# Kernel optimization log

Measured on AMD Instinct MI355X. Metric: run time of the kernel, lower is better.

## Reference

```python
import jax, jax.numpy as jnp
import numpy as np

N, E, IN, H, OUT = 50000, 800000, 128, 128, 64
BN_EPS = 1e-5


def setup_inputs() -> dict:
    key = jax.random.key(0)
    ks = jax.random.split(key, 12)
    x = jax.random.normal(ks[0], (N, IN), dtype=jnp.float32)
    edge_index = jax.random.randint(ks[1], (2, E), 0, N, dtype=jnp.int32)
    def lin(k, fan_in, fan_out):
        s = 1.0 / np.sqrt(fan_in)
        return jax.random.uniform(k, (fan_in, fan_out), jnp.float32, -s, s)
    params = {
        'W1': lin(ks[2], IN, H),  'b1': jnp.zeros((H,), jnp.float32),
        'W2': lin(ks[3], H, H),   'b2': jnp.zeros((H,), jnp.float32),
        'W3': lin(ks[4], H, H),   'b3': jnp.zeros((H,), jnp.float32),
        'W4': lin(ks[5], H, OUT), 'b4': jnp.zeros((OUT,), jnp.float32),
        'g1': jnp.ones((H,), jnp.float32), 'be1': jnp.zeros((H,), jnp.float32),
        'g2': jnp.ones((H,), jnp.float32), 'be2': jnp.zeros((H,), jnp.float32),
        'g3': jnp.ones((H,), jnp.float32), 'be3': jnp.zeros((H,), jnp.float32),
    }
    return dict(x=x, edge_index=edge_index, **params)


def _gcn_conv(x, src, dst, dinv, norm, W, b):
    # GCNConv: symmetric-normalized aggregation with self loops.
    h = x @ W                                   # [N, F]
    agg = jax.ops.segment_sum(h[src] * norm[:, None], dst, num_segments=N)
    agg = agg + h * (dinv * dinv)[:, None]      # self-loop contribution
    return agg + b


def _bn(x, gamma, beta):
    mu = jnp.mean(x, axis=0)
    var = jnp.mean(jnp.square(x - mu), axis=0)
    return (x - mu) * jax.lax.rsqrt(var + BN_EPS) * gamma + beta


def reference(x, edge_index, W1, b1, W2, b2, W3, b3, W4, b4, g1, be1, g2, be2, g3, be3):
    src, dst = edge_index[0], edge_index[1]
    # degree with self loops; fixed by the graph, shared across layers
    deg = jax.ops.segment_sum(jnp.ones((E,), x.dtype), dst, num_segments=N) + 1.0
    dinv = jax.lax.rsqrt(deg)
    norm = dinv[src] * dinv[dst]                # [E]

    h = _gcn_conv(x, src, dst, dinv, norm, W1, b1)
    h = jax.nn.relu(_bn(h, g1, be1))
    h = _gcn_conv(h, src, dst, dinv, norm, W2, b2)
    h = jax.nn.relu(_bn(h, g2, be2))
    h = _gcn_conv(h, src, dst, dinv, norm, W3, b3)
    h = jax.nn.relu(_bn(h, g3, be3))
    return _gcn_conv(h, src, dst, dinv, norm, W4, b4)
```

## Files before the change

kernel.cpp:

```cpp
#include <hip/hip_runtime.h>

constexpr int NN = 50000;
constexpr int NE = 800000;
constexpr float EPS = 1e-5f;

constexpr int CAP     = 64;
constexpr int FILL_NB = (NE + 255) / 256;
constexpr int WCONV_NB = (57344 + 255) / 256;

typedef short bf16x8 __attribute__((ext_vector_type(8)));
typedef float f32x4  __attribute__((ext_vector_type(4)));

__device__ __forceinline__ ushort f2bf(float x) {
    union { float f; unsigned u; } a; a.f = x;
    unsigned u = a.u;
    unsigned r = (u + 0x7FFFu + ((u >> 16) & 1u)) >> 16;
    return (ushort)r;
}
__device__ __forceinline__ float bflo(unsigned p) {
    union { unsigned u; float f; } a; a.u = p << 16; return a.f;
}
__device__ __forceinline__ float bfhi(unsigned p) {
    union { unsigned u; float f; } a; a.u = p & 0xFFFF0000u; return a.f;
}

__global__ void fillwconv_kernel(const int* __restrict__ src, const int* __restrict__ dst,
                                 int* __restrict__ curA, int* __restrict__ curB,
                                 ushort* __restrict__ csrf,
                                 const float* __restrict__ W1, const float* __restrict__ W2,
                                 const float* __restrict__ W3, const float* __restrict__ W4,
                                 ushort* __restrict__ Wt) {
    if (blockIdx.x < FILL_NB) {
        int e = blockIdx.x * 256 + threadIdx.x;
        if (e < NE) {
            int d = dst[e];
            if (e < NE / 2) {
                int slot = atomicAdd(&curA[d], 1);
                if (slot < CAP) csrf[(size_t)d * CAP + slot] = (ushort)src[e];
            } else {
                int old = atomicAdd(&curB[d], 1);
                int slot = CAP - 1 - old;
                if (slot >= 0) csrf[(size_t)d * CAP + slot] = (ushort)src[e];
            }
        }
    } else {
        int id = (blockIdx.x - FILL_NB) * 256 + threadIdx.x;
        if (id < 49152) {
            int l = id / 16384, r = id % 16384;
            int n = r >> 7, k = r & 127;
            const float* W = (l == 0) ? W1 : (l == 1) ? W2 : W3;
            Wt[l * 16384 + n * 128 + k] = f2bf(W[k * 128 + n]);
        } else if (id < 57344) {
            int r = id - 49152;
            int n = r >> 7, k = r & 127;
            Wt[49152 + n * 128 + k] = f2bf(W4[k * 64 + n]);
        }
    }
}

template<int F, bool BN>
__global__ __launch_bounds__(256, 3) void gemm_bf16_kernel(
    const void* __restrict__ Xv, const ushort* __restrict__ Wt,
    const int* __restrict__ curA, const int* __restrict__ curB,
    const float* __restrict__ sums, const float* __restrict__ sumsq,
    const float* __restrict__ g, const float* __restrict__ be,
    ushort* __restrict__ U)
{
    constexpr int NTW = F / 32;
    constexpr int LDK = 136;
    __shared__ __align__(16) ushort Xs[64 * LDK];
    __shared__ float scs[128], shs[128];

    const int tid  = threadIdx.x;
    const int wave = tid >> 6;
    const int lane = tid & 63;
    const int m    = lane & 15;
    const int q    = lane >> 4;
    const int rowHalf = wave & 1;
    const int colHalf = wave >> 1;
    const int row0 = blockIdx.x * 64;

    if constexpr (BN) {
        if (tid < 128) {
            float mu  = sums[tid] * (1.0f / NN);
            float var = sumsq[tid] * (1.0f / NN) - mu * mu;
            float scv = rsqrtf(var + EPS) * g[tid];
            scs[tid] = scv;
            shs[tid] = be[tid] - mu * scv;
        }
        __syncthreads();
    }

    bf16x8 w[NTW][4];
#pragma unroll
    for (int nt = 0; nt < NTW; nt++)
#pragma unroll
        for (int ks = 0; ks < 4; ks++)
            w[nt][ks] = *(const bf16x8*)&Wt[(colHalf * (F / 2) + nt * 16 + m) * 128 + ks * 32 + q * 8];

#pragma unroll
    for (int it = 0; it < 8; it++) {
        int idx = it * 256 + tid;
        int r   = idx >> 5;
        int c4  = (idx & 31) * 4;
        int row = row0 + r;
        float4 v = make_float4(0.f, 0.f, 0.f, 0.f);
        if constexpr (BN) {
            if (row < NN) {
                uint2 p = *(const uint2*)&((const ushort*)Xv)[(size_t)row * 128 + c4];
                v.x = bflo(p.x); v.y = bfhi(p.x);
                v.z = bflo(p.y); v.w = bfhi(p.y);
            }
            float4 s = *(const float4*)&scs[c4];
            float4 h = *(const float4*)&shs[c4];
            v.x = fmaxf(0.f, v.x * s.x + h.x);
            v.y = fmaxf(0.f, v.y * s.y + h.y);
            v.z = fmaxf(0.f, v.z * s.z + h.z);
            v.w = fmaxf(0.f, v.w * s.w + h.w);
        } else {
            if (row < NN) v = *(const float4*)&((const float*)Xv)[(size_t)row * 128 + c4];
        }
        ushort4 o;
        o.x = f2bf(v.x); o.y = f2bf(v.y); o.z = f2bf(v.z); o.w = f2bf(v.w);
        *(ushort4*)&Xs[r * LDK + c4] = o;
    }
    __syncthreads();

    f32x4 acc[2][NTW];
#pragma unroll
    for (int t = 0; t < 2; t++)
#pragma unroll
        for (int nt = 0; nt < NTW; nt++) acc[t][nt] = (f32x4){0.f, 0.f, 0.f, 0.f};

#pragma unroll
    for (int ks = 0; ks < 4; ks++) {
        bf16x8 a0 = *(const bf16x8*)&Xs[(rowHalf * 32 + m)      * LDK + ks * 32 + q * 8];
        bf16x8 a1 = *(const bf16x8*)&Xs[(rowHalf * 32 + 16 + m) * LDK + ks * 32 + q * 8];
#pragma unroll
        for (int nt = 0; nt < NTW; nt++) {
            acc[0][nt] = __builtin_amdgcn_mfma_f32_16x16x32_bf16(a0, w[nt][ks], acc[0][nt], 0, 0, 0);
            acc[1][nt] = __builtin_amdgcn_mfma_f32_16x16x32_bf16(a1, w[nt][ks], acc[1][nt], 0, 0, 0);
        }
    }

#pragma unroll
    for (int t = 0; t < 2; t++) {
#pragma unroll
        for (int r = 0; r < 4; r++) {
            int row = row0 + rowHalf * 32 + t * 16 + q * 4 + r;
            if (row < NN) {
                float di = rsqrtf((float)(curA[row] + curB[row]) + 1.0f);
#pragma unroll
                for (int nt = 0; nt < NTW; nt++) {
                    U[(size_t)row * F + colHalf * (F / 2) + nt * 16 + m] = f2bf(acc[t][nt][r] * di);
                }
            }
        }
    }
}

__global__ __launch_bounds__(256) void gather128_kernel(
    const ushort* __restrict__ csrf,
    const int* __restrict__ curA, const int* __restrict__ curB,
    const ushort* __restrict__ U, const float* __restrict__ b,
    ushort* __restrict__ Yb)
{
    int n    = (blockIdx.x * 256 + threadIdx.x) >> 6;
    int lane = threadIdx.x & 63;
    if (n >= NN) return;
    const int half = lane >> 5;
    const int c4   = (lane & 31) * 4;
    int dA = curA[n], dB = curB[n];
    int degRaw = dA + dB;
    int dA_c = min(dA, CAP);
    int dB_c = min(dB, CAP - dA_c);
    int myIdx = (int)csrf[(size_t)n * CAP + lane];
    float a0 = 0.f, a1 = 0.f, a2 = 0.f, a3 = 0.f;

    int j = 0;
    for (; j + 4 <= dA_c; j += 4) {
        int s0 = __shfl(myIdx, j + half);
        int s1 = __shfl(myIdx, j + 2 + half);
        uint2 u0 = *(const uint2*)&U[(size_t)s0 * 128 + c4];
        uint2 u1 = *(const uint2*)&U[(size_t)s1 * 128 + c4];
        a0 += bflo(u0.x) + bflo(u1.x);
        a1 += bfhi(u0.x) + bfhi(u1.x);
        a2 += bflo(u0.y) + bflo(u1.y);
        a3 += bfhi(u0.y) + bfhi(u1.y);
    }
    for (; j < dA_c; j += 2) {
        int jj = j + half;
        int s = __shfl(myIdx, min(jj, dA_c - 1));
        uint2 u = *(const uint2*)&U[(size_t)s * 128 + c4];
        if (jj < dA_c) {
            a0 += bflo(u.x); a1 += bfhi(u.x);
            a2 += bflo(u.y); a3 += bfhi(u.y);
        }
    }
    j = CAP - dB_c;
    for (; j + 4 <= CAP; j += 4) {
        int s0 = __shfl(myIdx, j + half);
        int s1 = __shfl(myIdx, j + 2 + half);
        uint2 u0 = *(const uint2*)&U[(size_t)s0 * 128 + c4];
        uint2 u1 = *(const uint2*)&U[(size_t)s1 * 128 + c4];
        a0 += bflo(u0.x) + bflo(u1.x);
        a1 += bfhi(u0.x) + bfhi(u1.x);
        a2 += bflo(u0.y) + bflo(u1.y);
        a3 += bfhi(u0.y) + bfhi(u1.y);
    }
    for (; j < CAP; j += 2) {
        int jj = j + half;
        int s = __shfl(myIdx, min(jj, CAP - 1));
        uint2 u = *(const uint2*)&U[(size_t)s * 128 + c4];
        if (jj < CAP) {
            a0 += bflo(u.x); a1 += bfhi(u.x);
            a2 += bflo(u.y); a3 += bfhi(u.y);
        }
    }

    a0 += __shfl_xor(a0, 32);
    a1 += __shfl_xor(a1, 32);
    a2 += __shfl_xor(a2, 32);
    a3 += __shfl_xor(a3, 32);

    uint2 us = *(const uint2*)&U[(size_t)n * 128 + c4];
    float di = rsqrtf((float)degRaw + 1.0f);
    float4 bb = *(const float4*)&b[c4];
    float o0 = di * (a0 + bflo(us.x)) + bb.x;
    float o1 = di * (a1 + bfhi(us.x)) + bb.y;
    float o2 = di * (a2 + bflo(us.y)) + bb.z;
    float o3 = di * (a3 + bfhi(us.y)) + bb.w;
    if (half == 0) {
        ushort4 o;
        o.x = f2bf(o0); o.y = f2bf(o1); o.z = f2bf(o2); o.w = f2bf(o3);
        *(ushort4*)&Yb[(size_t)n * 128 + c4] = o;
    }
}

__global__ __launch_bounds__(256) void gather64_kernel(
    const ushort* __restrict__ csrf,
    const int* __restrict__ curA, const int* __restrict__ curB,
    const ushort* __restrict__ U, const float* __restrict__ b,
    float* __restrict__ Y)
{
    int t  = blockIdx.x * 256 + threadIdx.x;
    int n  = t >> 5;
    int l2 = t & 31;
    if (n >= NN) return;
    const int coff = l2 * 2;
    int dA = curA[n], dB = curB[n];
    int degRaw = dA + dB;
    int dA_c = min(dA, CAP);
    int dB_c = min(dB, CAP - dA_c);
    int iA = (int)csrf[(size_t)n * CAP + l2];
    int iB = (int)csrf[(size_t)n * CAP + 32 + l2];
    float ax = 0.f, ay = 0.f;

    for (int j = 0; j < dA_c; j++) {
        int sl = __shfl(iA, j & 31, 32);
        int sh = __shfl(iB, j & 31, 32);
        int s  = (j < 32) ? sl : sh;
        unsigned u = *(const unsigned*)&U[(size_t)s * 64 + coff];
        ax += bflo(u); ay += bfhi(u);
    }
    for (int j = CAP - dB_c; j < CAP; j++) {
        int sl = __shfl(iA, j & 31, 32);
        int sh = __shfl(iB, j & 31, 32);
        int s  = (j < 32) ? sl : sh;
        unsigned u = *(const unsigned*)&U[(size_t)s * 64 + coff];
        ax += bflo(u); ay += bfhi(u);
    }

    unsigned us = *(const unsigned*)&U[(size_t)n * 64 + coff];
    float di = rsqrtf((float)degRaw + 1.0f);
    float ox = di * (ax + bflo(us)) + b[coff];
    float oy = di * (ay + bfhi(us)) + b[coff + 1];
    *(float2*)&Y[(size_t)n * 64 + coff] = make_float2(ox, oy);
}

__global__ __launch_bounds__(256) void stats_kernel(const ushort* __restrict__ Yb,
                                                    float* __restrict__ sums,
                                                    float* __restrict__ sumsq)
{
    __shared__ float ssum[128], ssq[128];
    if (threadIdx.x < 128) { ssum[threadIdx.x] = 0.f; ssq[threadIdx.x] = 0.f; }
    __syncthreads();

    const int lane   = threadIdx.x & 63;
    const int gwave  = (blockIdx.x * 256 + threadIdx.x) >> 6;
    const int nWaves = gridDim.x * 4;
    const int coff   = lane * 2;

    float s0 = 0.f, s1 = 0.f, q0 = 0.f, q1 = 0.f;
    for (int row = gwave; row < NN; row += nWaves) {
        unsigned p = *(const unsigned*)&Yb[(size_t)row * 128 + coff];
        float yx = bflo(p), yy = bfhi(p);
        s0 += yx; q0 += yx * yx;
        s1 += yy; q1 += yy * yy;
    }
    atomicAdd(&ssum[coff], s0);     atomicAdd(&ssum[coff + 1], s1);
    atomicAdd(&ssq[coff], q0);      atomicAdd(&ssq[coff + 1], q1);
    __syncthreads();
    if (threadIdx.x < 128) {
        atomicAdd(&sums[threadIdx.x],  ssum[threadIdx.x]);
        atomicAdd(&sumsq[threadIdx.x], ssq[threadIdx.x]);
    }
}

extern "C" void kernel_launch(void* const* d_in, const int* in_sizes, int n_in,
                              void* d_out, int out_size, void* d_ws, size_t ws_size,
                              hipStream_t stream)
{
    const float* x   = (const float*)d_in[0];
    const int*   ei  = (const int*)d_in[1];
    const int*   src = ei;
    const int*   dst = ei + NE;
    const float* W1 = (const float*)d_in[2];  const float* b1 = (const float*)d_in[3];
    const float* W2 = (const float*)d_in[4];  const float* b2 = (const float*)d_in[5];
    const float* W3 = (const float*)d_in[6];  const float* b3 = (const float*)d_in[7];
    const float* W4 = (const float*)d_in[8];  const float* b4 = (const float*)d_in[9];
    const float* g1 = (const float*)d_in[10]; const float* be1 = (const float*)d_in[11];
    const float* g2 = (const float*)d_in[12]; const float* be2 = (const float*)d_in[13];
    const float* g3 = (const float*)d_in[14]; const float* be3 = (const float*)d_in[15];
    float* out = (float*)d_out;

    char* wsb = (char*)d_ws;
    int*   curA   = (int*)wsb;
    int*   curB   = curA + NN;
    float* stats  = (float*)(curB + NN);
    ushort* Wt    = (ushort*)(stats + 768);
    ushort* csrf  = Wt + 57344;
    ushort* Yb    = csrf + (size_t)NN * CAP;
    ushort* U     = Yb + (size_t)NN * 128;

    float* sums1 = stats;       float* sumsq1 = stats + 128;
    float* sums2 = stats + 256; float* sumsq2 = stats + 384;
    float* sums3 = stats + 512; float* sumsq3 = stats + 640;

    const ushort* Wt1 = Wt;
    const ushort* Wt2 = Wt + 16384;
    const ushort* Wt3 = Wt + 32768;
    const ushort* Wt4 = Wt + 49152;

    const int gemmGrid   = (NN + 63) / 64;
    const int gathGrid   = (NN * 64 + 255) / 256;
    const int gath64Grid = (NN * 32 + 255) / 256;

    hipMemsetAsync(curA, 0, 2 * NN * sizeof(int) + 768 * sizeof(float), stream);
    fillwconv_kernel<<<FILL_NB + WCONV_NB, 256, 0, stream>>>(src, dst, curA, curB, csrf,
                                                             W1, W2, W3, W4, Wt);

    gemm_bf16_kernel<128, false><<<gemmGrid, 256, 0, stream>>>(x, Wt1, curA, curB, nullptr, nullptr, nullptr, nullptr, U);
    gather128_kernel<<<gathGrid, 256, 0, stream>>>(csrf, curA, curB, U, b1, Yb);
    stats_kernel<<<512, 256, 0, stream>>>(Yb, sums1, sumsq1);

    gemm_bf16_kernel<128, true><<<gemmGrid, 256, 0, stream>>>(Yb, Wt2, curA, curB, sums1, sumsq1, g1, be1, U);
    gather128_kernel<<<gathGrid, 256, 0, stream>>>(csrf, curA, curB, U, b2, Yb);
    stats_kernel<<<512, 256, 0, stream>>>(Yb, sums2, sumsq2);

    gemm_bf16_kernel<128, true><<<gemmGrid, 256, 0, stream>>>(Yb, Wt3, curA, curB, sums2, sumsq2, g2, be2, U);
    gather128_kernel<<<gathGrid, 256, 0, stream>>>(csrf, curA, curB, U, b3, Yb);
    stats_kernel<<<512, 256, 0, stream>>>(Yb, sums3, sumsq3);

    gemm_bf16_kernel<64, true><<<gemmGrid, 256, 0, stream>>>(Yb, Wt4, curA, curB, sums3, sumsq3, g3, be3, U);
    gather64_kernel<<<gath64Grid, 256, 0, stream>>>(csrf, curA, curB, U, b4, out);
}
```

Measured before the change: 397.1 us.

## Fuse graph prep and first GEMM, move source degree scaling into gather

Merges the CSR fill and weight conversion kernel with the first-layer GEMM into one launch, interleaving 4 GEMM tiles with 17 fill blocks per group. The layer-1 GEMM no longer depends on degrees because it reads W1 directly from fp32 and writes unscaled U. The source-side D^-1/2 scaling moves into the first gather, which looks up each neighbor's degree and multiplies per edge. This removes one launch and one serialization point so the GEMM overlaps the atomic fill, at the cost of extra per-edge multiplies and degree loads in the first gather.

```diff
diff --git a/kernel.cpp b/kernel.cpp
--- a/kernel.cpp
+++ b/kernel.cpp
@@ -7,6 +7,10 @@
 constexpr int CAP     = 64;
 constexpr int FILL_NB = (NE + 255) / 256;
 constexpr int WCONV_NB = (57344 + 255) / 256;
+constexpr int GEMM1_NB = (NN + 63) / 64;
+
+constexpr int GROUPS   = 197;
+constexpr int FUSED_NB = GROUPS * 21;
 
 typedef short bf16x8 __attribute__((ext_vector_type(8)));
 typedef float f32x4  __attribute__((ext_vector_type(4)));
@@ -24,36 +28,119 @@
     union { unsigned u; float f; } a; a.u = p & 0xFFFF0000u; return a.f;
 }
 
-__global__ void fillwconv_kernel(const int* __restrict__ src, const int* __restrict__ dst,
-                                 int* __restrict__ curA, int* __restrict__ curB,
-                                 ushort* __restrict__ csrf,
-                                 const float* __restrict__ W1, const float* __restrict__ W2,
-                                 const float* __restrict__ W3, const float* __restrict__ W4,
-                                 ushort* __restrict__ Wt) {
-    if (blockIdx.x < FILL_NB) {
-        int e = blockIdx.x * 256 + threadIdx.x;
-        if (e < NE) {
-            int d = dst[e];
-            if (e < NE / 2) {
-                int slot = atomicAdd(&curA[d], 1);
-                if (slot < CAP) csrf[(size_t)d * CAP + slot] = (ushort)src[e];
-            } else {
-                int old = atomicAdd(&curB[d], 1);
-                int slot = CAP - 1 - old;
-                if (slot >= 0) csrf[(size_t)d * CAP + slot] = (ushort)src[e];
+__global__ __launch_bounds__(256, 3) void fused_prep_gemm1(
+    const int* __restrict__ src, const int* __restrict__ dst,
+    int* __restrict__ curA, int* __restrict__ curB,
+    ushort* __restrict__ csrf,
+    const float* __restrict__ W1, const float* __restrict__ W2,
+    const float* __restrict__ W3, const float* __restrict__ W4,
+    ushort* __restrict__ Wt,
+    const float* __restrict__ X, ushort* __restrict__ U)
+{
+    constexpr int LDK = 136;
+    __shared__ __align__(16) ushort Xs[64 * LDK];
+
+    const int bx  = blockIdx.x;
+    const int g   = bx / 21;
+    const int l   = bx - g * 21;
+    const int tid = threadIdx.x;
+
+    if (l >= 4) {
+        int fid = g * 17 + (l - 4);
+        if (fid < FILL_NB) {
+            int e = fid * 256 + tid;
+            if (e < NE) {
+                int d = dst[e];
+                if (e < NE / 2) {
+                    int slot = atomicAdd(&curA[d], 1);
+                    if (slot < CAP) csrf[(size_t)d * CAP + slot] = (ushort)src[e];
+                } else {
+                    int old = atomicAdd(&curB[d], 1);
+                    int slot = CAP - 1 - old;
+                    if (slot >= 0) csrf[(size_t)d * CAP + slot] = (ushort)src[e];
+                }
             }
-        }
-    } else {
-        int id = (blockIdx.x - FILL_NB) * 256 + threadIdx.x;
-        if (id < 49152) {
-            int l = id / 16384, r = id % 16384;
-            int n = r >> 7, k = r & 127;
-            const float* W = (l == 0) ? W1 : (l == 1) ? W2 : W3;
-            Wt[l * 16384 + n * 128 + k] = f2bf(W[k * 128 + n]);
-        } else if (id < 57344) {
-            int r = id - 49152;
-            int n = r >> 7, k = r & 127;
-            Wt[49152 + n * 128 + k] = f2bf(W4[k * 64 + n]);
+        } else {
+            int id = (fid - FILL_NB) * 256 + tid;
+            if (id < 49152) {
+                int li = id / 16384, r = id % 16384;
+                int n = r >> 7, k = r & 127;
+                const float* W = (li == 0) ? W1 : (li == 1) ? W2 : W3;
+                Wt[li * 16384 + n * 128 + k] = f2bf(W[k * 128 + n]);
+            } else if (id < 57344) {
+                int r = id - 49152;
+                int n = r >> 7, k = r & 127;
+                Wt[49152 + n * 128 + k] = f2bf(W4[k * 64 + n]);
+            }
+        }
+        return;
+    }
+
+    int tile = g * 4 + l;
+    if (tile >= GEMM1_NB) return;
+
+    const int wave = tid >> 6;
+    const int lane = tid & 63;
+    const int m    = lane & 15;
+    const int q    = lane >> 4;
+    const int rowHalf = wave & 1;
+    const int colHalf = wave >> 1;
+    const int row0 = tile * 64;
+
+    bf16x8 w[4][4];
+#pragma unroll
+    for (int nt = 0; nt < 4; nt++) {
+#pragma unroll
+        for (int ks = 0; ks < 4; ks++) {
+            const float* wp = &W1[(ks * 32 + q * 8) * 128 + colHalf * 64 + nt * 16 + m];
+            bf16x8 t;
+#pragma unroll
+            for (int j = 0; j < 8; j++) t[j] = (short)f2bf(wp[j * 128]);
+            w[nt][ks] = t;
+        }
+    }
+
+#pragma unroll
+    for (int it = 0; it < 8; it++) {
+        int idx = it * 256 + tid;
+        int r   = idx >> 5;
+        int c4  = (idx & 31) * 4;
+        int row = row0 + r;
+        float4 v = make_float4(0.f, 0.f, 0.f, 0.f);
+        if (row < NN) v = *(const float4*)&X[(size_t)row * 128 + c4];
+        ushort4 o;
+        o.x = f2bf(v.x); o.y = f2bf(v.y); o.z = f2bf(v.z); o.w = f2bf(v.w);
+        *(ushort4*)&Xs[r * LDK + c4] = o;
+    }
+    __syncthreads();
+
+    f32x4 acc[2][4];
+#pragma unroll
+    for (int t = 0; t < 2; t++)
+#pragma unroll
+        for (int nt = 0; nt < 4; nt++) acc[t][nt] = (f32x4){0.f, 0.f, 0.f, 0.f};
+
+#pragma unroll
+    for (int ks = 0; ks < 4; ks++) {
+        bf16x8 a0 = *(const bf16x8*)&Xs[(rowHalf * 32 + m)      * LDK + ks * 32 + q * 8];
+        bf16x8 a1 = *(const bf16x8*)&Xs[(rowHalf * 32 + 16 + m) * LDK + ks * 32 + q * 8];
+#pragma unroll
+        for (int nt = 0; nt < 4; nt++) {
+            acc[0][nt] = __builtin_amdgcn_mfma_f32_16x16x32_bf16(a0, w[nt][ks], acc[0][nt], 0, 0, 0);
+            acc[1][nt] = __builtin_amdgcn_mfma_f32_16x16x32_bf16(a1, w[nt][ks], acc[1][nt], 0, 0, 0);
+        }
+    }
+
+#pragma unroll
+    for (int t = 0; t < 2; t++) {
+#pragma unroll
+        for (int r = 0; r < 4; r++) {
+            int row = row0 + rowHalf * 32 + t * 16 + q * 4 + r;
+            if (row < NN) {
+#pragma unroll
+                for (int nt = 0; nt < 4; nt++)
+                    U[(size_t)row * 128 + colHalf * 64 + nt * 16 + m] = f2bf(acc[t][nt][r]);
+            }
         }
     }
 }
@@ -159,6 +246,7 @@
     }
 }
 
+template<bool SRCSCALE>
 __global__ __launch_bounds__(256) void gather128_kernel(
     const ushort* __restrict__ csrf,
     const int* __restrict__ curA, const int* __restrict__ curB,
@@ -175,6 +263,11 @@
     int dA_c = min(dA, CAP);
     int dB_c = min(dB, CAP - dA_c);
     int myIdx = (int)csrf[(size_t)n * CAP + lane];
+    float myDs = 0.f;
+    if constexpr (SRCSCALE) {
+        int mi = min(myIdx, NN - 1);
+        myDs = rsqrtf((float)(curA[mi] + curB[mi]) + 1.0f);
+    }
     float a0 = 0.f, a1 = 0.f, a2 = 0.f, a3 = 0.f;
 
     int j = 0;
@@ -183,18 +276,30 @@
         int s1 = __shfl(myIdx, j + 2 + half);
         uint2 u0 = *(const uint2*)&U[(size_t)s0 * 128 + c4];
         uint2 u1 = *(const uint2*)&U[(size_t)s1 * 128 + c4];
-        a0 += bflo(u0.x) + bflo(u1.x);
-        a1 += bfhi(u0.x) + bfhi(u1.x);
-        a2 += bflo(u0.y) + bflo(u1.y);
-        a3 += bfhi(u0.y) + bfhi(u1.y);
+        if constexpr (SRCSCALE) {
+            float sc0 = __shfl(myDs, j + half);
+            float sc1 = __shfl(myDs, j + 2 + half);
+            a0 += sc0 * bflo(u0.x) + sc1 * bflo(u1.x);
+            a1 += sc0 * bfhi(u0.x) + sc1 * bfhi(u1.x);
+            a2 += sc0 * bflo(u0.y) + sc1 * bflo(u1.y);
+            a3 += sc0 * bfhi(u0.y) + sc1 * bfhi(u1.y);
+        } else {
+            a0 += bflo(u0.x) + bflo(u1.x);
+            a1 += bfhi(u0.x) + bfhi(u1.x);
+            a2 += bflo(u0.y) + bflo(u1.y);
+            a3 += bfhi(u0.y) + bfhi(u1.y);
+        }
     }
     for (; j < dA_c; j += 2) {
         int jj = j + half;
-        int s = __shfl(myIdx, min(jj, dA_c - 1));
+        int sl = min(jj, dA_c - 1);
+        int s  = __shfl(myIdx, sl);
+        float sc = 1.f;
+        if constexpr (SRCSCALE) sc = __shfl(myDs, sl);
         uint2 u = *(const uint2*)&U[(size_t)s * 128 + c4];
         if (jj < dA_c) {
-            a0 += bflo(u.x); a1 += bfhi(u.x);
-            a2 += bflo(u.y); a3 += bfhi(u.y);
+            a0 += sc * bflo(u.x); a1 += sc * bfhi(u.x);
+            a2 += sc * bflo(u.y); a3 += sc * bfhi(u.y);
         }
     }
     j = CAP - dB_c;
@@ -203,18 +308,30 @@
         int s1 = __shfl(myIdx, j + 2 + half);
         uint2 u0 = *(const uint2*)&U[(size_t)s0 * 128 + c4];
         uint2 u1 = *(const uint2*)&U[(size_t)s1 * 128 + c4];
-        a0 += bflo(u0.x) + bflo(u1.x);
-        a1 += bfhi(u0.x) + bfhi(u1.x);
-        a2 += bflo(u0.y) + bflo(u1.y);
-        a3 += bfhi(u0.y) + bfhi(u1.y);
+        if constexpr (SRCSCALE) {
+            float sc0 = __shfl(myDs, j + half);
+            float sc1 = __shfl(myDs, j + 2 + half);
+            a0 += sc0 * bflo(u0.x) + sc1 * bflo(u1.x);
+            a1 += sc0 * bfhi(u0.x) + sc1 * bfhi(u1.x);
+            a2 += sc0 * bflo(u0.y) + sc1 * bflo(u1.y);
+            a3 += sc0 * bfhi(u0.y) + sc1 * bfhi(u1.y);
+        } else {
+            a0 += bflo(u0.x) + bflo(u1.x);
+            a1 += bfhi(u0.x) + bfhi(u1.x);
+            a2 += bflo(u0.y) + bflo(u1.y);
+            a3 += bfhi(u0.y) + bfhi(u1.y);
+        }
     }
     for (; j < CAP; j += 2) {
         int jj = j + half;
-        int s = __shfl(myIdx, min(jj, CAP - 1));
+        int sl = min(jj, CAP - 1);
+        int s  = __shfl(myIdx, sl);
+        float sc = 1.f;
+        if constexpr (SRCSCALE) sc = __shfl(myDs, sl);
         uint2 u = *(const uint2*)&U[(size_t)s * 128 + c4];
         if (jj < CAP) {
-            a0 += bflo(u.x); a1 += bfhi(u.x);
-            a2 += bflo(u.y); a3 += bfhi(u.y);
+            a0 += sc * bflo(u.x); a1 += sc * bfhi(u.x);
+            a2 += sc * bflo(u.y); a3 += sc * bfhi(u.y);
         }
     }
 
@@ -225,11 +342,12 @@
 
     uint2 us = *(const uint2*)&U[(size_t)n * 128 + c4];
     float di = rsqrtf((float)degRaw + 1.0f);
+    float selfs = SRCSCALE ? di : 1.0f;
     float4 bb = *(const float4*)&b[c4];
-    float o0 = di * (a0 + bflo(us.x)) + bb.x;
-    float o1 = di * (a1 + bfhi(us.x)) + bb.y;
-    float o2 = di * (a2 + bflo(us.y)) + bb.z;
-    float o3 = di * (a3 + bfhi(us.y)) + bb.w;
+    float o0 = di * (a0 + selfs * bflo(us.x)) + bb.x;
+    float o1 = di * (a1 + selfs * bfhi(us.x)) + bb.y;
+    float o2 = di * (a2 + selfs * bflo(us.y)) + bb.z;
+    float o3 = di * (a3 + selfs * bfhi(us.y)) + bb.w;
     if (half == 0) {
         ushort4 o;
         o.x = f2bf(o0); o.y = f2bf(o1); o.z = f2bf(o2); o.w = f2bf(o3);
@@ -337,7 +455,6 @@
     float* sums2 = stats + 256; float* sumsq2 = stats + 384;
     float* sums3 = stats + 512; float* sumsq3 = stats + 640;
 
-    const ushort* Wt1 = Wt;
     const ushort* Wt2 = Wt + 16384;
     const ushort* Wt3 = Wt + 32768;
     const ushort* Wt4 = Wt + 49152;
@@ -347,19 +464,18 @@
     const int gath64Grid = (NN * 32 + 255) / 256;
 
     hipMemsetAsync(curA, 0, 2 * NN * sizeof(int) + 768 * sizeof(float), stream);
-    fillwconv_kernel<<<FILL_NB + WCONV_NB, 256, 0, stream>>>(src, dst, curA, curB, csrf,
-                                                             W1, W2, W3, W4, Wt);
-
-    gemm_bf16_kernel<128, false><<<gemmGrid, 256, 0, stream>>>(x, Wt1, curA, curB, nullptr, nullptr, nullptr, nullptr, U);
-    gather128_kernel<<<gathGrid, 256, 0, stream>>>(csrf, curA, curB, U, b1, Yb);
+    fused_prep_gemm1<<<FUSED_NB, 256, 0, stream>>>(src, dst, curA, curB, csrf,
+                                                   W1, W2, W3, W4, Wt, x, U);
+
+    gather128_kernel<true><<<gathGrid, 256, 0, stream>>>(csrf, curA, curB, U, b1, Yb);
     stats_kernel<<<512, 256, 0, stream>>>(Yb, sums1, sumsq1);
 
     gemm_bf16_kernel<128, true><<<gemmGrid, 256, 0, stream>>>(Yb, Wt2, curA, curB, sums1, sumsq1, g1, be1, U);
-    gather128_kernel<<<gathGrid, 256, 0, stream>>>(csrf, curA, curB, U, b2, Yb);
+    gather128_kernel<false><<<gathGrid, 256, 0, stream>>>(csrf, curA, curB, U, b2, Yb);
     stats_kernel<<<512, 256, 0, stream>>>(Yb, sums2, sumsq2);
 
     gemm_bf16_kernel<128, true><<<gemmGrid, 256, 0, stream>>>(Yb, Wt3, curA, curB, sums2, sumsq2, g2, be2, U);
-    gather128_kernel<<<gathGrid, 256, 0, stream>>>(csrf, curA, curB, U, b3, Yb);
+    gather128_kernel<false><<<gathGrid, 256, 0, stream>>>(csrf, curA, curB, U, b3, Yb);
     stats_kernel<<<512, 256, 0, stream>>>(Yb, sums3, sumsq3);
 
     gemm_bf16_kernel<64, true><<<gemmGrid, 256, 0, stream>>>(Yb, Wt4, curA, curB, sums3, sumsq3, g3, be3, U);
```

Result: no change. 392.5 us (-1.2%).
